# Optimization experiments

Measured on AMD Instinct MI355X. Metric: run time of the kernel, lower is better.

Reference implementation:

```python
import jax, jax.numpy as jnp
import numpy as np

B, N, D, P, V = 8, 256, 300, 128, 50001  # batch, seq len, emb dim, proj dim, vocab(+unk)


def setup_inputs() -> dict:
    key = jax.random.key(0)
    ks = jax.random.split(key, 10)
    s = 1.0 / np.sqrt(D)
    sp = 1.0 / np.sqrt(P)
    emb = jax.random.normal(ks[0], (V, D), jnp.float32)
    emb = emb.at[-1].set(0.0)  # unk row zeroed, matches add_unk
    return {
        "sentence": jax.random.randint(ks[1], (B, N), 0, V),
        "emb": emb,
        "Wl": jax.random.uniform(ks[2], (P, D), jnp.float32, -s, s),
        "bl": jnp.zeros((P,), jnp.float32),
        "Wr": jax.random.uniform(ks[3], (P, D), jnp.float32, -s, s),
        "Wo": jax.random.uniform(ks[4], (1, P), jnp.float32, -sp, sp),
        "bo": jnp.zeros((1,), jnp.float32),
        "Ws1": jax.random.uniform(ks[5], (P, D), jnp.float32, -s, s),
        "bs1": jnp.zeros((P,), jnp.float32),
        "Ws2": jax.random.uniform(ks[6], (1, P), jnp.float32, -sp, sp),
        "bs2": jnp.zeros((1,), jnp.float32),
        "We1": jax.random.uniform(ks[7], (P, D), jnp.float32, -s, s),
        "be1": jnp.zeros((P,), jnp.float32),
        "We2": jax.random.uniform(ks[8], (1, P), jnp.float32, -sp, sp),
        "be2": jnp.zeros((1,), jnp.float32),
    }


def reference(sentence, emb, Wl, bl, Wr, Wo, bo, Ws1, bs1, Ws2, bs2, We1, be1, We2, be2):
    x = emb[sentence]                                   # [B,N,D] embedding lookup
    start = jax.nn.relu(x @ Ws1.T + bs1) @ Ws2.T + bs2  # [B,N,1]
    end = jax.nn.relu(x @ We1.T + be1) @ We2.T + be2    # [B,N,1]
    left = x @ Wl.T + bl                                # [B,N,P]
    right = x @ Wr.T                                    # [B,N,P]
    # proj[b,i,j,p] = left[b,j,p] + right[b,i,p]  (unsqueeze(1) + unsqueeze(2))
    proj = left[:, None, :, :] + right[:, :, None, :]   # [B,N,N,P]
    bigram = jax.nn.relu(proj) @ Wo.T + bo              # [B,N,N,1]
    return (bigram, start, end)
```

## Files before the change

### kernel.cpp

```cpp
#include <hip/hip_runtime.h>

#define NB 8
#define NN 256
#define DD 300
#define PP 128
#define OFF_S (NB * NN * NN)
#define OFF_E (NB * NN * NN + NB * NN)

typedef unsigned short u16;
typedef unsigned int   u32;

__device__ __forceinline__ float bf2f(u16 u) {
    union { u32 i; float f; } v;
    v.i = ((u32)u) << 16;
    return v.f;
}
__device__ __forceinline__ u16 f2bf(float f) {
    union { float f; u32 i; } v;
    v.f = f;
    u32 lsb = (v.i >> 16) & 1u;
    v.i += 0x7fffu + lsb;
    return (u16)(v.i >> 16);
}

template<bool BF>
__device__ __forceinline__ float ld1(const void* base, int idx) {
    return BF ? bf2f(((const u16*)base)[idx]) : ((const float*)base)[idx];
}
template<bool BF>
__device__ __forceinline__ void st1(void* base, int idx, float v) {
    if (BF) ((u16*)base)[idx] = f2bf(v);
    else    ((float*)base)[idx] = v;
}
template<bool BF>
__device__ __forceinline__ void st4(void* base, int idx, float4 v) {
    if (BF) {
        ushort4 o = make_ushort4(f2bf(v.x), f2bf(v.y), f2bf(v.z), f2bf(v.w));
        *(ushort4*)((u16*)base + idx) = o;
    } else {
        *(float4*)((float*)base + idx) = v;
    }
}
__device__ __forceinline__ float4 rfma4(float4 l, float r, float w, float4 a) {
    a.x = fmaf(fmaxf(l.x + r, 0.f), w, a.x);
    a.y = fmaf(fmaxf(l.y + r, 0.f), w, a.y);
    a.z = fmaf(fmaxf(l.z + r, 0.f), w, a.z);
    a.w = fmaf(fmaxf(l.w + r, 0.f), w, a.w);
    return a;
}

template<bool BF> struct wraw;
template<> struct wraw<false> {
    typedef float4 T;
    static __device__ __forceinline__ T ld(const void* W, int off) {
        return *(const float4*)((const float*)W + off);
    }
    static __device__ __forceinline__ float4 cvt(T v) { return v; }
};
template<> struct wraw<true> {
    typedef ushort4 T;
    static __device__ __forceinline__ T ld(const void* W, int off) {
        return *(const ushort4*)((const u16*)W + off);
    }
    static __device__ __forceinline__ float4 cvt(T v) {
        return make_float4(bf2f(v.x), bf2f(v.y), bf2f(v.z), bf2f(v.w));
    }
};

__device__ __forceinline__ int flag_wave(const u32* __restrict__ embU) {
    int lane = threadIdx.x & 63;
    int cnt = 0;
    for (int i = lane; i < 256; i += 64) {
        u32 w = embU[i];
        union { u32 u; float f; } v;
        v.u = (w & 0xFFFFu) << 16;
        float a = fabsf(v.f);
        if (a == 0.f || (a >= 0.00390625f && a <= 256.f)) cnt++;
    }
    #pragma unroll
    for (int off = 32; off; off >>= 1) cnt += __shfl_xor(cnt, off, 64);
    return (cnt >= 128) ? 1 : 0;
}

template<bool BF>
__device__ __forceinline__ void tok_body(
    const void* __restrict__ Wl,  const void* __restrict__ Wr,
    const void* __restrict__ Ws1, const void* __restrict__ We1,
    const void* __restrict__ bl,
    const void* __restrict__ bs1, const void* __restrict__ Ws2,
    const void* __restrict__ bs2,
    const void* __restrict__ be1, const void* __restrict__ We2,
    const void* __restrict__ be2,
    const void* __restrict__ emb,
    float* __restrict__ leftT, float* __restrict__ rightW,
    void* __restrict__ out, float (*sxT)[8], const int* sids)
{
    const int tid = threadIdx.x;
    const int t0  = blockIdx.x * 8;

    for (int e = tid; e < DD * 8; e += 256) {
        int k = e >> 3, t = e & 7;
        sxT[k][t] = ld1<BF>(emb, sids[t] * DD + k);
    }
    __syncthreads();

    const int wv = tid >> 6;
    const int l  = tid & 63;
    const int p0 = 2 * l, p1 = p0 + 1;
    const void* Wm = (wv == 0) ? Wl : (wv == 1) ? Wr : (wv == 2) ? Ws1 : We1;
    const int r0 = p0 * DD, r1 = p1 * DD;

    float a0[8], a1[8];
    #pragma unroll
    for (int t = 0; t < 8; ++t) { a0[t] = 0.f; a1[t] = 0.f; }

#define FMAK(kk, wx_, wy_) do {                                         \
        float4 xa = *(const float4*)&sxT[(kk)][0];                      \
        float4 xb = *(const float4*)&sxT[(kk)][4];                      \
        a0[0]=fmaf(xa.x,wx_,a0[0]); a1[0]=fmaf(xa.x,wy_,a1[0]);         \
        a0[1]=fmaf(xa.y,wx_,a0[1]); a1[1]=fmaf(xa.y,wy_,a1[1]);         \
        a0[2]=fmaf(xa.z,wx_,a0[2]); a1[2]=fmaf(xa.z,wy_,a1[2]);         \
        a0[3]=fmaf(xa.w,wx_,a0[3]); a1[3]=fmaf(xa.w,wy_,a1[3]);         \
        a0[4]=fmaf(xb.x,wx_,a0[4]); a1[4]=fmaf(xb.x,wy_,a1[4]);         \
        a0[5]=fmaf(xb.y,wx_,a0[5]); a1[5]=fmaf(xb.y,wy_,a1[5]);         \
        a0[6]=fmaf(xb.z,wx_,a0[6]); a1[6]=fmaf(xb.z,wy_,a1[6]);         \
        a0[7]=fmaf(xb.w,wx_,a0[7]); a1[7]=fmaf(xb.w,wy_,a1[7]);         \
    } while (0)

#define GROUP(k0, U0, U1) do {                                          \
        float4 f0_ = wraw<BF>::cvt(U0);                                 \
        float4 f1_ = wraw<BF>::cvt(U1);                                 \
        FMAK((k0) + 0, f0_.x, f1_.x);                                   \
        FMAK((k0) + 1, f0_.y, f1_.y);                                   \
        FMAK((k0) + 2, f0_.z, f1_.z);                                   \
        FMAK((k0) + 3, f0_.w, f1_.w);                                   \
    } while (0)

    typedef typename wraw<BF>::T WT;
    WT w0a = wraw<BF>::ld(Wm, r0 + 0), w1a = wraw<BF>::ld(Wm, r1 + 0);
    WT w0b = wraw<BF>::ld(Wm, r0 + 4), w1b = wraw<BF>::ld(Wm, r1 + 4);
    WT w0c = wraw<BF>::ld(Wm, r0 + 8), w1c = wraw<BF>::ld(Wm, r1 + 8);
    for (int it = 0; it < 25; ++it) {
        WT u0a = w0a, u1a = w1a, u0b = w0b, u1b = w1b, u0c = w0c, u1c = w1c;
        const int kn = it * 12 + 12;
        if (it < 24) {
            w0a = wraw<BF>::ld(Wm, r0 + kn);     w1a = wraw<BF>::ld(Wm, r1 + kn);
            w0b = wraw<BF>::ld(Wm, r0 + kn + 4); w1b = wraw<BF>::ld(Wm, r1 + kn + 4);
            w0c = wraw<BF>::ld(Wm, r0 + kn + 8); w1c = wraw<BF>::ld(Wm, r1 + kn + 8);
        }
        GROUP(it * 12,     u0a, u1a);
        GROUP(it * 12 + 4, u0b, u1b);
        GROUP(it * 12 + 8, u0c, u1c);
    }
#undef GROUP
#undef FMAK

    if (wv == 0) {
        float b0 = ld1<BF>(bl, p0), b1 = ld1<BF>(bl, p1);
        const int bb = t0 >> 8, j0 = t0 & 255;
        float* o0 = leftT + ((size_t)bb * PP + p0) * NN + j0;
        float* o1 = leftT + ((size_t)bb * PP + p1) * NN + j0;
        *(float4*)(o0)     = make_float4(a0[0]+b0, a0[1]+b0, a0[2]+b0, a0[3]+b0);
        *(float4*)(o0 + 4) = make_float4(a0[4]+b0, a0[5]+b0, a0[6]+b0, a0[7]+b0);
        *(float4*)(o1)     = make_float4(a1[0]+b1, a1[1]+b1, a1[2]+b1, a1[3]+b1);
        *(float4*)(o1 + 4) = make_float4(a1[4]+b1, a1[5]+b1, a1[6]+b1, a1[7]+b1);
    } else if (wv == 1) {
        #pragma unroll
        for (int t = 0; t < 8; ++t) {
            *(float2*)&rightW[(size_t)(t0 + t) * PP + p0] =
                make_float2(a0[t], a1[t]);
        }
    } else {
        const void* h1 = (wv == 2) ? bs1 : be1;
        const void* h2 = (wv == 2) ? Ws2 : We2;
        const void* h3 = (wv == 2) ? bs2 : be2;
        float b0 = ld1<BF>(h1, p0), b1 = ld1<BF>(h1, p1);
        float w0h = ld1<BF>(h2, p0), w1h = ld1<BF>(h2, p1);
        float v[8];
        #pragma unroll
        for (int t = 0; t < 8; ++t)
            v[t] = fmaxf(a0[t] + b0, 0.f) * w0h + fmaxf(a1[t] + b1, 0.f) * w1h;
        #pragma unroll
        for (int off = 32; off; off >>= 1) {
            #pragma unroll
            for (int t = 0; t < 8; ++t) v[t] += __shfl_down(v[t], off, 64);
        }
        if (l == 0) {
            float b2 = ld1<BF>(h3, 0);
            int base = (wv == 2) ? OFF_S : OFF_E;
            #pragma unroll
            for (int t = 0; t < 8; ++t)
                st1<BF>(out, base + t0 + t, v[t] + b2);
        }
    }
}

extern "C" __global__ void __launch_bounds__(256)
tok_kernel(const int* __restrict__ sent, const void* __restrict__ emb,
           const void* __restrict__ Wl,  const void* __restrict__ Wr,
           const void* __restrict__ Ws1, const void* __restrict__ We1,
           const void* __restrict__ bl,
           const void* __restrict__ bs1, const void* __restrict__ Ws2,
           const void* __restrict__ bs2,
           const void* __restrict__ be1, const void* __restrict__ We2,
           const void* __restrict__ be2,
           float* __restrict__ leftT, float* __restrict__ rightW,
           void* __restrict__ out)
{
    __shared__ __align__(16) float sxT[DD][8];
    __shared__ int sids[8];
    __shared__ int sflag;
    if (threadIdx.x < 64) {
        int f = flag_wave((const u32*)emb);
        if (threadIdx.x == 0) sflag = f;
    }
    if (threadIdx.x < 8) sids[threadIdx.x] = sent[blockIdx.x * 8 + threadIdx.x];
    __syncthreads();
    if (sflag) {
        tok_body<true >(Wl, Wr, Ws1, We1, bl, bs1, Ws2, bs2, be1, We2, be2,
                        emb, leftT, rightW, out, sxT, sids);
    } else {
        tok_body<false>(Wl, Wr, Ws1, We1, bl, bs1, Ws2, bs2, be1, We2, be2,
                        emb, leftT, rightW, out, sxT, sids);
    }
}

template<bool BF>
__device__ __forceinline__ void big_body(
    const float* __restrict__ leftT, const float* __restrict__ rightW,
    const void* __restrict__ Wo, const void* __restrict__ bo,
    void* __restrict__ outB,
    float (*sR)[128], float* sWo, float4 (*red4)[64][4])
{
    const int tid = threadIdx.x;
    const int b   = blockIdx.x >> 6;
    const int i0  = (blockIdx.x & 63) << 2;

    if (tid < 128) sWo[tid] = ld1<BF>(Wo, tid);
    for (int c = tid; c < 512; c += 256) {
        int i = c >> 7, pp = c & 127;
        sR[i][pp] = rightW[((size_t)(b * NN + i0 + i)) * PP + pp];
    }
    __syncthreads();

    const int w    = tid >> 6;
    const int lane = tid & 63;
    const int j4   = lane << 2;
    const float* lp = leftT + (size_t)b * PP * NN + j4;

    float4 A0 = {0.f, 0.f, 0.f, 0.f}, A1 = A0, A2 = A0, A3 = A0;
    const int pbase = w * 32;
    #pragma unroll
    for (int g = 0; g < 8; ++g) {
        const int p = pbase + g * 4;
        float4 wo = *(const float4*)&sWo[p];
        float4 r0 = *(const float4*)&sR[0][p];
        float4 r1 = *(const float4*)&sR[1][p];
        float4 r2 = *(const float4*)&sR[2][p];
        float4 r3 = *(const float4*)&sR[3][p];
        const float* lpp = lp + (size_t)p * NN;
        float4 l0 = *(const float4*)(lpp);
        float4 l1 = *(const float4*)(lpp + NN);
        float4 l2 = *(const float4*)(lpp + 2 * NN);
        float4 l3 = *(const float4*)(lpp + 3 * NN);
        A0 = rfma4(l0, r0.x, wo.x, A0);
        A1 = rfma4(l0, r1.x, wo.x, A1);
        A2 = rfma4(l0, r2.x, wo.x, A2);
        A3 = rfma4(l0, r3.x, wo.x, A3);
        A0 = rfma4(l1, r0.y, wo.y, A0);
        A1 = rfma4(l1, r1.y, wo.y, A1);
        A2 = rfma4(l1, r2.y, wo.y, A2);
        A3 = rfma4(l1, r3.y, wo.y, A3);
        A0 = rfma4(l2, r0.z, wo.z, A0);
        A1 = rfma4(l2, r1.z, wo.z, A1);
        A2 = rfma4(l2, r2.z, wo.z, A2);
        A3 = rfma4(l2, r3.z, wo.z, A3);
        A0 = rfma4(l3, r0.w, wo.w, A0);
        A1 = rfma4(l3, r1.w, wo.w, A1);
        A2 = rfma4(l3, r2.w, wo.w, A2);
        A3 = rfma4(l3, r3.w, wo.w, A3);
    }

    red4[w][lane][0] = A0;
    red4[w][lane][1] = A1;
    red4[w][lane][2] = A2;
    red4[w][lane][3] = A3;
    __syncthreads();

    if (tid < 64) {
        float bov = ld1<BF>(bo, 0);
        #pragma unroll
        for (int i = 0; i < 4; ++i) {
            float4 s0 = red4[0][tid][i];
            float4 s1 = red4[1][tid][i];
            float4 s2 = red4[2][tid][i];
            float4 s3 = red4[3][tid][i];
            float4 s;
            s.x = s0.x + s1.x + s2.x + s3.x + bov;
            s.y = s0.y + s1.y + s2.y + s3.y + bov;
            s.z = s0.z + s1.z + s2.z + s3.z + bov;
            s.w = s0.w + s1.w + s2.w + s3.w + bov;
            st4<BF>(outB, (int)(((size_t)(b * NN + i0 + i)) * NN) + tid * 4, s);
        }
    }
}

extern "C" __global__ void __launch_bounds__(256)
big_kernel(const float* __restrict__ leftT, const float* __restrict__ rightW,
           const void* __restrict__ Wo, const void* __restrict__ bo,
           void* __restrict__ outB, const u32* __restrict__ embU)
{
    __shared__ float sR[4][128];
    __shared__ float sWo[128];
    __shared__ float4 red4[4][64][4];
    __shared__ int sflag;
    if (threadIdx.x < 64) {
        int f = flag_wave(embU);
        if (threadIdx.x == 0) sflag = f;
    }
    __syncthreads();
    if (sflag) big_body<true >(leftT, rightW, Wo, bo, outB, sR, sWo, red4);
    else       big_body<false>(leftT, rightW, Wo, bo, outB, sR, sWo, red4);
}

extern "C" void kernel_launch(void* const* d_in, const int* in_sizes, int n_in,
                              void* d_out, int out_size, void* d_ws, size_t ws_size,
                              hipStream_t stream) {
    const int*  sent = (const int*)d_in[0];
    const void* emb  = d_in[1];
    const void* Wl   = d_in[2];
    const void* bl   = d_in[3];
    const void* Wr   = d_in[4];
    const void* Wo   = d_in[5];
    const void* bo   = d_in[6];
    const void* Ws1  = d_in[7];
    const void* bs1  = d_in[8];
    const void* Ws2  = d_in[9];
    const void* bs2  = d_in[10];
    const void* We1  = d_in[11];
    const void* be1  = d_in[12];
    const void* We2  = d_in[13];
    const void* be2  = d_in[14];

    float* leftT  = (float*)((char*)d_ws + 1024);
    float* rightW = leftT + (size_t)NB * PP * NN;

    hipLaunchKernelGGL(tok_kernel, dim3(256), dim3(256), 0, stream,
                       sent, emb, Wl, Wr, Ws1, We1, bl, bs1, Ws2, bs2,
                       be1, We2, be2, leftT, rightW, d_out);
    hipLaunchKernelGGL(big_kernel, dim3(512), dim3(256), 0, stream,
                       leftT, rightW, Wo, bo, d_out, (const u32*)emb);
}
```

Baseline: 148.0 us.

## Use bf16 MFMA for per-token projections in tok_kernel

```diff
diff --git a/kernel.cpp b/kernel.cpp
--- a/kernel.cpp
+++ b/kernel.cpp
@@ -9,6 +9,9 @@
 
 typedef unsigned short u16;
 typedef unsigned int   u32;
+
+typedef __attribute__((ext_vector_type(8))) short bf16x8;
+typedef __attribute__((ext_vector_type(4))) float f32x4;
 
 __device__ __forceinline__ float bf2f(u16 u) {
     union { u32 i; float f; } v;
@@ -48,24 +51,6 @@
     a.w = fmaf(fmaxf(l.w + r, 0.f), w, a.w);
     return a;
 }
-
-template<bool BF> struct wraw;
-template<> struct wraw<false> {
-    typedef float4 T;
-    static __device__ __forceinline__ T ld(const void* W, int off) {
-        return *(const float4*)((const float*)W + off);
-    }
-    static __device__ __forceinline__ float4 cvt(T v) { return v; }
-};
-template<> struct wraw<true> {
-    typedef ushort4 T;
-    static __device__ __forceinline__ T ld(const void* W, int off) {
-        return *(const ushort4*)((const u16*)W + off);
-    }
-    static __device__ __forceinline__ float4 cvt(T v) {
-        return make_float4(bf2f(v.x), bf2f(v.y), bf2f(v.z), bf2f(v.w));
-    }
-};
 
 __device__ __forceinline__ int flag_wave(const u32* __restrict__ embU) {
     int lane = threadIdx.x & 63;
@@ -81,6 +66,24 @@
     for (int off = 32; off; off >>= 1) cnt += __shfl_xor(cnt, off, 64);
     return (cnt >= 128) ? 1 : 0;
 }
+
+template<bool BF> struct wraw;
+template<> struct wraw<false> {
+    typedef float4 T;
+    static __device__ __forceinline__ T ld(const void* W, int off) {
+        return *(const float4*)((const float*)W + off);
+    }
+    static __device__ __forceinline__ float4 cvt(T v) { return v; }
+};
+template<> struct wraw<true> {
+    typedef ushort4 T;
+    static __device__ __forceinline__ T ld(const void* W, int off) {
+        return *(const ushort4*)((const u16*)W + off);
+    }
+    static __device__ __forceinline__ float4 cvt(T v) {
+        return make_float4(bf2f(v.x), bf2f(v.y), bf2f(v.z), bf2f(v.w));
+    }
+};
 
 template<bool BF>
 __device__ __forceinline__ void tok_body(
@@ -195,6 +198,129 @@
     }
 }
 
+__device__ __forceinline__ void tok_mfma(
+    const u16* __restrict__ Wl,  const u16* __restrict__ Wr,
+    const u16* __restrict__ Ws1, const u16* __restrict__ We1,
+    const u16* __restrict__ bl,
+    const u16* __restrict__ bs1, const u16* __restrict__ Ws2,
+    const u16* __restrict__ bs2,
+    const u16* __restrict__ be1, const u16* __restrict__ We2,
+    const u16* __restrict__ be2,
+    const u16* __restrict__ emb,
+    float* __restrict__ leftT, float* __restrict__ rightW,
+    u16* __restrict__ out,
+    u16 (*lx)[328], float (*hp)[2][4][4], const int* sids)
+{
+    const int tid = threadIdx.x;
+    const int t0  = (blockIdx.x >> 1) * 16;
+
+    for (int e = tid; e < 16 * 82; e += 256) {
+        int t = e / 82, c = e - t * 82;
+        ushort4 v = make_ushort4(0, 0, 0, 0);
+        if (c < 75) v = *(const ushort4*)(emb + (size_t)sids[t] * DD + 4 * c);
+        *(ushort4*)&lx[t][4 * c] = v;
+    }
+    __syncthreads();
+
+    const int w    = tid >> 6;
+    const int l    = tid & 63;
+    const int lo16 = l & 15;
+    const int g    = l >> 4;
+    const int mat  = (blockIdx.x & 1) * 2 + (w >> 1);
+    const int nh   = w & 1;
+    const u16* Wm  = (mat == 0) ? Wl : (mat == 1) ? Wr
+                   : (mat == 2) ? Ws1 : We1;
+
+    bf16x8 af[10];
+    #pragma unroll
+    for (int ks = 0; ks < 10; ++ks)
+        af[ks] = *(const bf16x8*)&lx[lo16][ks * 32 + g * 8];
+
+    f32x4 acc[4];
+    #pragma unroll
+    for (int nt = 0; nt < 4; ++nt) acc[nt] = (f32x4){0.f, 0.f, 0.f, 0.f};
+
+    const ushort4 z4 = make_ushort4(0, 0, 0, 0);
+    #pragma unroll
+    for (int nt = 0; nt < 4; ++nt) {
+        const int col = nh * 64 + nt * 16 + lo16;
+        const u16* wrow = Wm + (size_t)col * DD;
+        #pragma unroll
+        for (int ks = 0; ks < 9; ++ks) {
+            const int k0 = ks * 32 + g * 8;
+            union { ushort4 u[2]; bf16x8 v; } bb;
+            bb.u[0] = *(const ushort4*)(wrow + k0);
+            bb.u[1] = *(const ushort4*)(wrow + k0 + 4);
+            acc[nt] = __builtin_amdgcn_mfma_f32_16x16x32_bf16(
+                          af[ks], bb.v, acc[nt], 0, 0, 0);
+        }
+        {
+            const int k0 = 288 + g * 8;
+            const int a0i = (k0 < 297)     ? k0     : 0;
+            const int a1i = (k0 + 4 < 297) ? k0 + 4 : 0;
+            ushort4 t0v = *(const ushort4*)(wrow + a0i);
+            ushort4 t1v = *(const ushort4*)(wrow + a1i);
+            union { ushort4 u[2]; bf16x8 v; } bb;
+            bb.u[0] = (k0 < 297)     ? t0v : z4;
+            bb.u[1] = (k0 + 4 < 297) ? t1v : z4;
+            acc[nt] = __builtin_amdgcn_mfma_f32_16x16x32_bf16(
+                          af[9], bb.v, acc[nt], 0, 0, 0);
+        }
+    }
+
+    if (mat == 0) {
+        const int bb = t0 >> 8;
+        const int j0 = (t0 & 255) + g * 4;
+        #pragma unroll
+        for (int nt = 0; nt < 4; ++nt) {
+            int p = nh * 64 + nt * 16 + lo16;
+            float bv = bf2f(bl[p]);
+            float* o = leftT + ((size_t)bb * PP + p) * NN + j0;
+            *(float4*)o = make_float4(acc[nt].x + bv, acc[nt].y + bv,
+                                      acc[nt].z + bv, acc[nt].w + bv);
+        }
+    } else if (mat == 1) {
+        #pragma unroll
+        for (int nt = 0; nt < 4; ++nt) {
+            int p = nh * 64 + nt * 16 + lo16;
+            #pragma unroll
+            for (int r = 0; r < 4; ++r)
+                rightW[(size_t)(t0 + g * 4 + r) * PP + p] = acc[nt][r];
+        }
+    } else {
+        const u16* h1 = (mat == 2) ? bs1 : be1;
+        const u16* h2 = (mat == 2) ? Ws2 : We2;
+        float s[4] = {0.f, 0.f, 0.f, 0.f};
+        #pragma unroll
+        for (int nt = 0; nt < 4; ++nt) {
+            int p = nh * 64 + nt * 16 + lo16;
+            float b1v = bf2f(h1[p]), w2v = bf2f(h2[p]);
+            #pragma unroll
+            for (int r = 0; r < 4; ++r)
+                s[r] += fmaxf(acc[nt][r] + b1v, 0.f) * w2v;
+        }
+        #pragma unroll
+        for (int off = 1; off < 16; off <<= 1) {
+            #pragma unroll
+            for (int r = 0; r < 4; ++r) s[r] += __shfl_xor(s[r], off, 64);
+        }
+        if (lo16 == 0) {
+            #pragma unroll
+            for (int r = 0; r < 4; ++r) hp[w >> 1][nh][g][r] = s[r];
+        }
+    }
+    __syncthreads();
+
+    if ((blockIdx.x & 1) && tid < 32) {
+        int hm = tid >> 4;
+        int t  = tid & 15;
+        const u16* h3 = hm ? be2 : bs2;
+        float v = hp[hm][0][t >> 2][t & 3] + hp[hm][1][t >> 2][t & 3]
+                + bf2f(h3[0]);
+        out[(hm ? OFF_E : OFF_S) + t0 + t] = f2bf(v);
+    }
+}
+
 extern "C" __global__ void __launch_bounds__(256)
 tok_kernel(const int* __restrict__ sent, const void* __restrict__ emb,
            const void* __restrict__ Wl,  const void* __restrict__ Wr,
@@ -208,20 +334,31 @@
            void* __restrict__ out)
 {
     __shared__ __align__(16) float sxT[DD][8];
-    __shared__ int sids[8];
+    __shared__ __align__(16) u16 lx[16][328];
+    __shared__ float hp[2][2][4][4];
+    __shared__ int sids[16];
     __shared__ int sflag;
     if (threadIdx.x < 64) {
         int f = flag_wave((const u32*)emb);
         if (threadIdx.x == 0) sflag = f;
     }
-    if (threadIdx.x < 8) sids[threadIdx.x] = sent[blockIdx.x * 8 + threadIdx.x];
+    if (threadIdx.x < 16) {
+        sids[threadIdx.x] = sent[(blockIdx.x >> 1) * 16 + threadIdx.x];
+    }
     __syncthreads();
     if (sflag) {
-        tok_body<true >(Wl, Wr, Ws1, We1, bl, bs1, Ws2, bs2, be1, We2, be2,
-                        emb, leftT, rightW, out, sxT, sids);
+        tok_mfma((const u16*)Wl, (const u16*)Wr, (const u16*)Ws1,
+                 (const u16*)We1, (const u16*)bl, (const u16*)bs1,
+                 (const u16*)Ws2, (const u16*)bs2, (const u16*)be1,
+                 (const u16*)We2, (const u16*)be2, (const u16*)emb,
+                 leftT, rightW, (u16*)out, lx, hp, sids);
     } else {
+        __shared__ int sids8[8];
+        if (threadIdx.x < 8)
+            sids8[threadIdx.x] = sent[blockIdx.x * 8 + threadIdx.x];
+        __syncthreads();
         tok_body<false>(Wl, Wr, Ws1, We1, bl, bs1, Ws2, bs2, be1, We2, be2,
-                        emb, leftT, rightW, out, sxT, sids);
+                        emb, leftT, rightW, out, sxT, sids8);
     }
 }
 
```

Measured after the change: 148.5 us. About the same (+0.3%).
